# Performance work log

Measured on AMD Instinct MI355X. Metric: run time of the kernel, lower is better.

## Reference

```python
import jax, jax.numpy as jnp
import numpy as np

BATCH, IN_DIM, OUT_DIM = 4096, 8192, 16384

# Each of the 16 logic gates is affine in {1, a, b, a*b}. Rows below give the
# coefficients (const, a, b, ab) for gate k, matching the torch `gate` match-case.
_GATE_COEFS = np.array([
    [0, 0, 0, 0],    # 0: zeros
    [0, 0, 0, 1],    # 1: a*b
    [0, 1, 0, -1],   # 2: a - a*b
    [0, 1, 0, 0],    # 3: a
    [0, 0, 1, -1],   # 4: b - a*b
    [0, 0, 1, 0],    # 5: b
    [0, 1, 1, -2],   # 6: a + b - 2ab (xor)
    [0, 1, 1, -1],   # 7: a + b - ab (or)
    [1, -1, -1, 1],  # 8: 1 - (a + b - ab) (nor)
    [1, -1, -1, 2],  # 9: 1 - (a + b - 2ab) (xnor)
    [1, 0, -1, 0],   # 10: 1 - b
    [1, 0, -1, 1],   # 11: 1 - b + ab
    [1, -1, 0, 0],   # 12: 1 - a
    [1, -1, 0, 1],   # 13: 1 - a + ab
    [1, 0, 0, -1],   # 14: 1 - ab (nand)
    [1, 0, 0, 0],    # 15: ones
], dtype=np.float32)


def setup_inputs() -> dict:
    key = jax.random.key(0)
    k1, k2, k3, k4 = jax.random.split(key, 4)
    x = jax.random.uniform(k1, (BATCH, IN_DIM), dtype=jnp.float32)
    weights = jax.random.normal(k2, (OUT_DIM, 16), dtype=jnp.float32)
    idx_a = jax.random.randint(k3, (OUT_DIM,), 0, IN_DIM, dtype=jnp.int32)
    idx_b = jax.random.randint(k4, (OUT_DIM,), 0, IN_DIM, dtype=jnp.int32)
    return {"x": x, "weights": weights, "idx_a": idx_a, "idx_b": idx_b}


def reference(x, weights, idx_a, idx_b):
    # Training path: softmax over the 16 gate logits per output neuron.
    w = jax.nn.softmax(weights, axis=-1)            # [O, 16]
    # Collapse the 16-gate weighted sum into 4 affine coefficients per neuron.
    coef = w @ jnp.asarray(_GATE_COEFS)             # [O, 4] -> (c0, ca, cb, cab)
    a = x[..., idx_a]                               # [B, O] gather
    b = x[..., idx_b]                               # [B, O] gather
    return coef[:, 0] + coef[:, 1] * a + coef[:, 2] * b + coef[:, 3] * (a * b)
```

## Files before the change

### kernel.cpp

```cpp
#include <hip/hip_runtime.h>
#include <cstddef>
#include <cstdint>

constexpr int BATCH   = 4096;
constexpr int IN_DIM  = 8192;
constexpr int OUT_DIM = 16384;
constexpr int THREADS = 256;
constexpr int NBLK    = BATCH / 2;
constexpr int OPT     = 4;
constexpr int ITERS   = OUT_DIM / (THREADS * OPT);
constexpr int SSTEPS  = (IN_DIM / 4) / THREADS;

typedef float    f32x4 __attribute__((ext_vector_type(4)));
typedef uint32_t u32x4 __attribute__((ext_vector_type(4)));

__device__ __forceinline__ uint32_t f2bf(float f) {
  uint32_t u = __float_as_uint(f);
  u += 0x7fffu + ((u >> 16) & 1u);
  return u >> 16;
}
__device__ __forceinline__ uint32_t pack_bf(float a, float b) {
  return f2bf(a) | (f2bf(b) << 16);
}
__device__ __forceinline__ float bf_lo(uint32_t u) { return __uint_as_float(u << 16); }
__device__ __forceinline__ float bf_hi(uint32_t u) { return __uint_as_float(u & 0xffff0000u); }

__global__ __launch_bounds__(64)
void coef_kernel(const float* __restrict__ weights,
                 const int* __restrict__ idx_a,
                 const int* __restrict__ idx_b,
                 float4* __restrict__ coef,
                 uint32_t* __restrict__ pidx) {
  const int o = blockIdx.x * 64 + threadIdx.x;
  if (o >= OUT_DIM) return;

  const float4* wp = reinterpret_cast<const float4*>(weights + (size_t)o * 16);
  float4 t0 = wp[0], t1 = wp[1], t2 = wp[2], t3 = wp[3];
  float w[16] = { t0.x, t0.y, t0.z, t0.w, t1.x, t1.y, t1.z, t1.w,
                  t2.x, t2.y, t2.z, t2.w, t3.x, t3.y, t3.z, t3.w };
  float m = w[0];
#pragma unroll
  for (int i = 1; i < 16; ++i) m = fmaxf(m, w[i]);
  float p[16]; float s = 0.f;
#pragma unroll
  for (int i = 0; i < 16; ++i) { p[i] = __expf(w[i] - m); s += p[i]; }
  const float inv = 1.0f / s;
  const float GC[16]  = {0,0,0,0, 0,0,0,0, 1,1,1,1, 1,1,1,1};
  const float GA[16]  = {0,0,1,1, 0,0,1,1, -1,-1,0,0, -1,-1,0,0};
  const float GB[16]  = {0,0,0,0, 1,1,1,1, -1,-1,-1,-1, 0,0,0,0};
  const float GAB[16] = {0,1,-1,0, -1,0,-2,-1, 1,2,0,1, 0,1,-1,0};
  float c0 = 0.f, ca = 0.f, cb = 0.f, cab = 0.f;
#pragma unroll
  for (int i = 0; i < 16; ++i) {
    c0 += p[i] * GC[i]; ca += p[i] * GA[i];
    cb += p[i] * GB[i]; cab += p[i] * GAB[i];
  }
  coef[o] = make_float4(c0 * inv, ca * inv, cb * inv, cab * inv);
  pidx[o] = (uint32_t)idx_a[o] | ((uint32_t)idx_b[o] << 16);
}

__global__ __launch_bounds__(THREADS)
void logic_main(const float* __restrict__ x,
                const float4* __restrict__ coef,
                const uint32_t* __restrict__ pidx,
                float* __restrict__ out) {
  __shared__ uint32_t xp[IN_DIM];

  const int t  = threadIdx.x;
  const int b0 = blockIdx.x * 2;

  const f32x4* __restrict__ r0 =
      reinterpret_cast<const f32x4*>(x + (size_t)b0 * IN_DIM);
  const f32x4* __restrict__ r1 =
      reinterpret_cast<const f32x4*>(x + (size_t)(b0 + 1) * IN_DIM);

#pragma unroll
  for (int s = 0; s < SSTEPS; ++s) {
    const int q = s * THREADS + t;
    f32x4 a = r0[q];
    f32x4 b = r1[q];
    u32x4 pk;
    pk.x = pack_bf(a.x, b.x);
    pk.y = pack_bf(a.y, b.y);
    pk.z = pack_bf(a.z, b.z);
    pk.w = pack_bf(a.w, b.w);
    *reinterpret_cast<u32x4*>(&xp[4 * q]) = pk;
  }
  __syncthreads();

#pragma unroll 4
  for (int it = 0; it < ITERS; ++it) {
    const int o = it * (THREADS * OPT) + t * OPT;

    const int4 pi = *reinterpret_cast<const int4*>(pidx + o);
    const float4 c0 = coef[o + 0], c1 = coef[o + 1],
                 c2 = coef[o + 2], c3 = coef[o + 3];

    const uint32_t ga0 = xp[(uint32_t)pi.x & 0xffffu], gb0 = xp[(uint32_t)pi.x >> 16];
    const uint32_t ga1 = xp[(uint32_t)pi.y & 0xffffu], gb1 = xp[(uint32_t)pi.y >> 16];
    const uint32_t ga2 = xp[(uint32_t)pi.z & 0xffffu], gb2 = xp[(uint32_t)pi.z >> 16];
    const uint32_t ga3 = xp[(uint32_t)pi.w & 0xffffu], gb3 = xp[(uint32_t)pi.w >> 16];

    f32x4 res0, res1;
    {
      const float a0 = bf_lo(ga0), b0v = bf_lo(gb0);
      const float a1 = bf_hi(ga0), b1v = bf_hi(gb0);
      res0.x = fmaf(fmaf(c0.w, a0, c0.z), b0v, fmaf(c0.y, a0, c0.x));
      res1.x = fmaf(fmaf(c0.w, a1, c0.z), b1v, fmaf(c0.y, a1, c0.x));
    }
    {
      const float a0 = bf_lo(ga1), b0v = bf_lo(gb1);
      const float a1 = bf_hi(ga1), b1v = bf_hi(gb1);
      res0.y = fmaf(fmaf(c1.w, a0, c1.z), b0v, fmaf(c1.y, a0, c1.x));
      res1.y = fmaf(fmaf(c1.w, a1, c1.z), b1v, fmaf(c1.y, a1, c1.x));
    }
    {
      const float a0 = bf_lo(ga2), b0v = bf_lo(gb2);
      const float a1 = bf_hi(ga2), b1v = bf_hi(gb2);
      res0.z = fmaf(fmaf(c2.w, a0, c2.z), b0v, fmaf(c2.y, a0, c2.x));
      res1.z = fmaf(fmaf(c2.w, a1, c2.z), b1v, fmaf(c2.y, a1, c2.x));
    }
    {
      const float a0 = bf_lo(ga3), b0v = bf_lo(gb3);
      const float a1 = bf_hi(ga3), b1v = bf_hi(gb3);
      res0.w = fmaf(fmaf(c3.w, a0, c3.z), b0v, fmaf(c3.y, a0, c3.x));
      res1.w = fmaf(fmaf(c3.w, a1, c3.z), b1v, fmaf(c3.y, a1, c3.x));
    }

    *reinterpret_cast<f32x4*>(out + (size_t)b0 * OUT_DIM + o) = res0;
    *reinterpret_cast<f32x4*>(out + (size_t)(b0 + 1) * OUT_DIM + o) = res1;
  }
}

extern "C" void kernel_launch(void* const* d_in, const int* in_sizes, int n_in,
                              void* d_out, int out_size, void* d_ws, size_t ws_size,
                              hipStream_t stream) {
  const float* x       = (const float*)d_in[0];
  const float* weights = (const float*)d_in[1];
  const int*   idx_a   = (const int*)d_in[2];
  const int*   idx_b   = (const int*)d_in[3];
  float*       out     = (float*)d_out;

  float4*   coef = (float4*)d_ws;
  uint32_t* pidx = (uint32_t*)((char*)d_ws + (size_t)OUT_DIM * 16);

  coef_kernel<<<OUT_DIM / 64, 64, 0, stream>>>(weights, idx_a, idx_b, coef, pidx);
  logic_main<<<NBLK, THREADS, 0, stream>>>(x, coef, pidx, out);
}
```

Before: 109.2 us.

## Process four batch rows per block and prefetch coefficients across chunks

Each block now stages four input rows into two bf16-packed shared tables and uses 512 threads. Every coefficient and index load is reused for four outputs instead of two, which halves the coef/pidx traffic per output. The next chunk's coefficients are loaded into registers before the current results are stored. LDS use per block doubles, which may cut the number of resident blocks per CU.

```diff
diff --git a/kernel.cpp b/kernel.cpp
--- a/kernel.cpp
+++ b/kernel.cpp
@@ -5,10 +5,11 @@
 constexpr int BATCH   = 4096;
 constexpr int IN_DIM  = 8192;
 constexpr int OUT_DIM = 16384;
-constexpr int THREADS = 256;
-constexpr int NBLK    = BATCH / 2;
+constexpr int THREADS = 512;
+constexpr int RPB     = 4;
+constexpr int NBLK    = BATCH / RPB;
 constexpr int OPT     = 4;
-constexpr int ITERS   = OUT_DIM / (THREADS * OPT);
+constexpr int CHUNKS  = OUT_DIM / (THREADS * OPT);
 constexpr int SSTEPS  = (IN_DIM / 4) / THREADS;
 
 typedef float    f32x4 __attribute__((ext_vector_type(4)));
@@ -59,76 +60,100 @@
   pidx[o] = (uint32_t)idx_a[o] | ((uint32_t)idx_b[o] << 16);
 }
 
+__device__ __forceinline__ float2 eval2(float4 c, uint32_t ga, uint32_t gb) {
+  const float a0 = bf_lo(ga), b0 = bf_lo(gb);
+  const float a1 = bf_hi(ga), b1 = bf_hi(gb);
+  float2 r;
+  r.x = fmaf(fmaf(c.w, a0, c.z), b0, fmaf(c.y, a0, c.x));
+  r.y = fmaf(fmaf(c.w, a1, c.z), b1, fmaf(c.y, a1, c.x));
+  return r;
+}
+
 __global__ __launch_bounds__(THREADS)
 void logic_main(const float* __restrict__ x,
                 const float4* __restrict__ coef,
                 const uint32_t* __restrict__ pidx,
                 float* __restrict__ out) {
-  __shared__ uint32_t xp[IN_DIM];
+  __shared__ uint32_t xpA[IN_DIM];
+  __shared__ uint32_t xpB[IN_DIM];
 
   const int t  = threadIdx.x;
-  const int b0 = blockIdx.x * 2;
+  const int b0 = blockIdx.x * RPB;
 
   const f32x4* __restrict__ r0 =
-      reinterpret_cast<const f32x4*>(x + (size_t)b0 * IN_DIM);
+      reinterpret_cast<const f32x4*>(x + (size_t)(b0 + 0) * IN_DIM);
   const f32x4* __restrict__ r1 =
       reinterpret_cast<const f32x4*>(x + (size_t)(b0 + 1) * IN_DIM);
+  const f32x4* __restrict__ r2 =
+      reinterpret_cast<const f32x4*>(x + (size_t)(b0 + 2) * IN_DIM);
+  const f32x4* __restrict__ r3 =
+      reinterpret_cast<const f32x4*>(x + (size_t)(b0 + 3) * IN_DIM);
+
+  int o0 = t * OPT;
+  int4   pi = *reinterpret_cast<const int4*>(pidx + o0);
+  float4 c0 = coef[o0 + 0], c1 = coef[o0 + 1],
+         c2 = coef[o0 + 2], c3 = coef[o0 + 3];
 
 #pragma unroll
   for (int s = 0; s < SSTEPS; ++s) {
     const int q = s * THREADS + t;
-    f32x4 a = r0[q];
-    f32x4 b = r1[q];
-    u32x4 pk;
-    pk.x = pack_bf(a.x, b.x);
-    pk.y = pack_bf(a.y, b.y);
-    pk.z = pack_bf(a.z, b.z);
-    pk.w = pack_bf(a.w, b.w);
-    *reinterpret_cast<u32x4*>(&xp[4 * q]) = pk;
+    f32x4 a = r0[q], b = r1[q];
+    u32x4 pkA;
+    pkA.x = pack_bf(a.x, b.x); pkA.y = pack_bf(a.y, b.y);
+    pkA.z = pack_bf(a.z, b.z); pkA.w = pack_bf(a.w, b.w);
+    *reinterpret_cast<u32x4*>(&xpA[4 * q]) = pkA;
+    f32x4 c = r2[q], d = r3[q];
+    u32x4 pkB;
+    pkB.x = pack_bf(c.x, d.x); pkB.y = pack_bf(c.y, d.y);
+    pkB.z = pack_bf(c.z, d.z); pkB.w = pack_bf(c.w, d.w);
+    *reinterpret_cast<u32x4*>(&xpB[4 * q]) = pkB;
   }
   __syncthreads();
 
-#pragma unroll 4
-  for (int it = 0; it < ITERS; ++it) {
-    const int o = it * (THREADS * OPT) + t * OPT;
+#pragma unroll 2
+  for (int ch = 0; ch < CHUNKS; ++ch) {
+    const int o = ch * (THREADS * OPT) + t * OPT;
 
-    const int4 pi = *reinterpret_cast<const int4*>(pidx + o);
-    const float4 c0 = coef[o + 0], c1 = coef[o + 1],
-                 c2 = coef[o + 2], c3 = coef[o + 3];
+    const uint32_t i0a = (uint32_t)pi.x & 0xffffu, i0b = (uint32_t)pi.x >> 16;
+    const uint32_t i1a = (uint32_t)pi.y & 0xffffu, i1b = (uint32_t)pi.y >> 16;
+    const uint32_t i2a = (uint32_t)pi.z & 0xffffu, i2b = (uint32_t)pi.z >> 16;
+    const uint32_t i3a = (uint32_t)pi.w & 0xffffu, i3b = (uint32_t)pi.w >> 16;
 
-    const uint32_t ga0 = xp[(uint32_t)pi.x & 0xffffu], gb0 = xp[(uint32_t)pi.x >> 16];
-    const uint32_t ga1 = xp[(uint32_t)pi.y & 0xffffu], gb1 = xp[(uint32_t)pi.y >> 16];
-    const uint32_t ga2 = xp[(uint32_t)pi.z & 0xffffu], gb2 = xp[(uint32_t)pi.z >> 16];
-    const uint32_t ga3 = xp[(uint32_t)pi.w & 0xffffu], gb3 = xp[(uint32_t)pi.w >> 16];
+    const uint32_t gA0a = xpA[i0a], gA0b = xpA[i0b];
+    const uint32_t gA1a = xpA[i1a], gA1b = xpA[i1b];
+    const uint32_t gA2a = xpA[i2a], gA2b = xpA[i2b];
+    const uint32_t gA3a = xpA[i3a], gA3b = xpA[i3b];
+    const uint32_t gB0a = xpB[i0a], gB0b = xpB[i0b];
+    const uint32_t gB1a = xpB[i1a], gB1b = xpB[i1b];
+    const uint32_t gB2a = xpB[i2a], gB2b = xpB[i2b];
+    const uint32_t gB3a = xpB[i3a], gB3b = xpB[i3b];
 
-    f32x4 res0, res1;
-    {
-      const float a0 = bf_lo(ga0), b0v = bf_lo(gb0);
-      const float a1 = bf_hi(ga0), b1v = bf_hi(gb0);
-      res0.x = fmaf(fmaf(c0.w, a0, c0.z), b0v, fmaf(c0.y, a0, c0.x));
-      res1.x = fmaf(fmaf(c0.w, a1, c0.z), b1v, fmaf(c0.y, a1, c0.x));
-    }
-    {
-      const float a0 = bf_lo(ga1), b0v = bf_lo(gb1);
-      const float a1 = bf_hi(ga1), b1v = bf_hi(gb1);
-      res0.y = fmaf(fmaf(c1.w, a0, c1.z), b0v, fmaf(c1.y, a0, c1.x));
-      res1.y = fmaf(fmaf(c1.w, a1, c1.z), b1v, fmaf(c1.y, a1, c1.x));
-    }
-    {
-      const float a0 = bf_lo(ga2), b0v = bf_lo(gb2);
-      const float a1 = bf_hi(ga2), b1v = bf_hi(gb2);
-      res0.z = fmaf(fmaf(c2.w, a0, c2.z), b0v, fmaf(c2.y, a0, c2.x));
-      res1.z = fmaf(fmaf(c2.w, a1, c2.z), b1v, fmaf(c2.y, a1, c2.x));
-    }
-    {
-      const float a0 = bf_lo(ga3), b0v = bf_lo(gb3);
-      const float a1 = bf_hi(ga3), b1v = bf_hi(gb3);
-      res0.w = fmaf(fmaf(c3.w, a0, c3.z), b0v, fmaf(c3.y, a0, c3.x));
-      res1.w = fmaf(fmaf(c3.w, a1, c3.z), b1v, fmaf(c3.y, a1, c3.x));
+    const float2 e00 = eval2(c0, gA0a, gA0b);
+    const float2 e01 = eval2(c1, gA1a, gA1b);
+    const float2 e02 = eval2(c2, gA2a, gA2b);
+    const float2 e03 = eval2(c3, gA3a, gA3b);
+    const float2 e10 = eval2(c0, gB0a, gB0b);
+    const float2 e11 = eval2(c1, gB1a, gB1b);
+    const float2 e12 = eval2(c2, gB2a, gB2b);
+    const float2 e13 = eval2(c3, gB3a, gB3b);
+
+    f32x4 res0, res1, res2, res3;
+    res0.x = e00.x; res0.y = e01.x; res0.z = e02.x; res0.w = e03.x;
+    res1.x = e00.y; res1.y = e01.y; res1.z = e02.y; res1.w = e03.y;
+    res2.x = e10.x; res2.y = e11.x; res2.z = e12.x; res2.w = e13.x;
+    res3.x = e10.y; res3.y = e11.y; res3.z = e12.y; res3.w = e13.y;
+
+    if (ch + 1 < CHUNKS) {
+      const int on = o + THREADS * OPT;
+      pi = *reinterpret_cast<const int4*>(pidx + on);
+      c0 = coef[on + 0]; c1 = coef[on + 1];
+      c2 = coef[on + 2]; c3 = coef[on + 3];
     }
 
-    *reinterpret_cast<f32x4*>(out + (size_t)b0 * OUT_DIM + o) = res0;
+    *reinterpret_cast<f32x4*>(out + (size_t)(b0 + 0) * OUT_DIM + o) = res0;
     *reinterpret_cast<f32x4*>(out + (size_t)(b0 + 1) * OUT_DIM + o) = res1;
+    *reinterpret_cast<f32x4*>(out + (size_t)(b0 + 2) * OUT_DIM + o) = res2;
+    *reinterpret_cast<f32x4*>(out + (size_t)(b0 + 3) * OUT_DIM + o) = res3;
   }
 }
 
```

Result: faster. 100.7 us (-7.8%).
